# Kernel tuning notes

Hardware: AMD Instinct MI355X
Metric: run time of the kernel (lower is better)

The kernel has to match this reference:

```python
import jax, jax.numpy as jnp
import numpy as np

H = 768
R = 7  # len(DISCOURSE_RELATIONS)


def setup_inputs() -> dict:
    key = jax.random.key(0)
    ks = jax.random.split(key, 6)
    B, S = 4, 256
    scale = 1.0 / np.sqrt(H)
    return {
        "pooled_outputs": jax.random.normal(ks[0], (B, S, H), dtype=jnp.float32),
        "w_src": jax.random.uniform(ks[1], (H, H), jnp.float32, -scale, scale),
        "b_src": jax.random.uniform(ks[2], (H,), jnp.float32, -scale, scale),
        "w_tgt": jax.random.uniform(ks[3], (H, H), jnp.float32, -scale, scale),
        "b_tgt": jax.random.uniform(ks[4], (H,), jnp.float32, -scale, scale),
        "w_out": jax.random.uniform(ks[5], (R, H), jnp.float32, -scale, scale),
    }


def reference(pooled_outputs, w_src, b_src, w_tgt, b_tgt, w_out):
    # h_src, h_tgt: [B, S, H]
    h_src = jnp.einsum("bsh,kh->bsk", pooled_outputs, w_src) + b_src
    h_tgt = jnp.einsum("bth,kh->btk", pooled_outputs, w_tgt) + b_tgt
    # broadcast add -> [B, S, S, H], tanh, then small-output linear -> [B, S, S, R]
    h = jnp.tanh(h_src[:, :, None, :] + h_tgt[:, None, :, :])
    return jnp.einsum("bsth,rh->bstr", h, w_out)
```

## Files before the change

kernel.cpp:

```cpp
#include <hip/hip_runtime.h>
#include <hip/hip_bf16.h>

#define HD 768
#define SQ 256
#define NB 4
#define RR 7

typedef short bf16x8 __attribute__((ext_vector_type(8)));
typedef float f32x4  __attribute__((ext_vector_type(4)));

__device__ __forceinline__ float fast_tanh(float x) {
  float e = __expf(2.0f * x);
  return 1.0f - 2.0f / (e + 1.0f);
}

__device__ __forceinline__ float pair_tanh(float a, float b) {
  return (a + b) * __builtin_amdgcn_rcpf(fmaf(a, b, 1.0f));
}

__device__ __forceinline__ short f2bf(float x) {
  return (short)__builtin_bit_cast(unsigned short, __float2bfloat16(x));
}

__device__ __forceinline__ void gl_lds16(const void* g, void* l) {
  __builtin_amdgcn_global_load_lds(
      (const __attribute__((address_space(1))) void*)g,
      (__attribute__((address_space(3))) void*)l, 16, 0, 0);
}

__global__ __launch_bounds__(256) void cvt_kernel(
    const float* __restrict__ X, const float* __restrict__ Ws,
    const float* __restrict__ Wt, const float* __restrict__ Wo,
    short* __restrict__ Xb, short* __restrict__ Wsb,
    short* __restrict__ Wtb, short* __restrict__ Wob)
{
  const int NX = NB * SQ * HD / 8;
  const int NW = HD * HD / 8;
  const int NO = 16 * HD / 8;
  int i = blockIdx.x * 256 + threadIdx.x;
  const float* src; short* dst;
  if (i < NX)               { src = X;  dst = Xb; }
  else if (i < NX + NW)     { src = Ws; dst = Wsb; i -= NX; }
  else if (i < NX + 2 * NW) { src = Wt; dst = Wtb; i -= NX + NW; }
  else if (i < NX + 2 * NW + NO) {
    i -= NX + 2 * NW;
    int row = i / (HD / 8);
    bf16x8 r = {};
    if (row < RR) {
      float4 a = *(const float4*)(Wo + (size_t)i * 8);
      float4 b = *(const float4*)(Wo + (size_t)i * 8 + 4);
      r[0] = f2bf(a.x); r[1] = f2bf(a.y); r[2] = f2bf(a.z); r[3] = f2bf(a.w);
      r[4] = f2bf(b.x); r[5] = f2bf(b.y); r[6] = f2bf(b.z); r[7] = f2bf(b.w);
    }
    *(bf16x8*)(Wob + (size_t)i * 8) = r;
    return;
  } else return;
  float4 a = *(const float4*)(src + (size_t)i * 8);
  float4 b = *(const float4*)(src + (size_t)i * 8 + 4);
  bf16x8 r;
  r[0] = f2bf(a.x); r[1] = f2bf(a.y); r[2] = f2bf(a.z); r[3] = f2bf(a.w);
  r[4] = f2bf(b.x); r[5] = f2bf(b.y); r[6] = f2bf(b.z); r[7] = f2bf(b.w);
  *(bf16x8*)(dst + (size_t)i * 8) = r;
}

__global__ __launch_bounds__(256) void cvt_wout(
    const float* __restrict__ Wo, short* __restrict__ Wob)
{
  const int NO = 16 * HD / 8;
  int i = blockIdx.x * 256 + threadIdx.x;
  if (i >= NO) return;
  int row = i / (HD / 8);
  bf16x8 r = {};
  if (row < RR) {
    float4 a = *(const float4*)(Wo + (size_t)i * 8);
    float4 b = *(const float4*)(Wo + (size_t)i * 8 + 4);
    r[0] = f2bf(a.x); r[1] = f2bf(a.y); r[2] = f2bf(a.z); r[3] = f2bf(a.w);
    r[4] = f2bf(b.x); r[5] = f2bf(b.y); r[6] = f2bf(b.z); r[7] = f2bf(b.w);
  }
  *(bf16x8*)(Wob + (size_t)i * 8) = r;
}

__global__ __launch_bounds__(256) void stage1_lds(
    const short* __restrict__ Xb,
    const short* __restrict__ Wsb, const float* __restrict__ bsrc,
    const short* __restrict__ Wtb, const float* __restrict__ btgt,
    float* __restrict__ ta, float* __restrict__ tb)
{
  constexpr int BK = 64, BM = 32, BN = 64;
  const short* W  = blockIdx.z ? Wtb : Wsb;
  const float* bv = blockIdx.z ? btgt : bsrc;
  float* outp     = blockIdx.z ? tb : ta;
  const int row0 = blockIdx.x * BM, col0 = blockIdx.y * BN;

  __shared__ short As[2][BM * BK];
  __shared__ short Bs[2][BN * BK];

  const int tid = threadIdx.x, wave = tid >> 6, lane = tid & 63;
  const int ln = lane & 15, lg = lane >> 4;
  const int wm = (wave >> 1) * 16, wn = (wave & 1) * 32;

  f32x4 acc[2] = {};

  const int ra = tid >> 3, ga = tid & 7;
  const size_t xoff = (size_t)(row0 + ra) * HD + ((ga ^ (ra & 7)) * 8);
  const int rb0 = tid >> 3, gb0 = tid & 7;
  const int rb1 = (tid + 256) >> 3, gb1 = tid & 7;
  const size_t wof0 = (size_t)(col0 + rb0) * HD + ((gb0 ^ (rb0 & 7)) * 8);
  const size_t wof1 = (size_t)(col0 + rb1) * HD + ((gb1 ^ (rb1 & 7)) * 8);
  short* const laA  = (short*)As + (size_t)(wave * 64) * 8;
  short* const laB0 = (short*)Bs + (size_t)(wave * 64) * 8;
  short* const laB1 = (short*)Bs + (size_t)(256 + wave * 64) * 8;
  constexpr int BUFA = BM * BK, BUFB = BN * BK;

  gl_lds16(Xb + xoff, laA);
  gl_lds16(W + wof0, laB0);
  gl_lds16(W + wof1, laB1);

  int cur = 0;
  for (int k0 = 0; k0 < HD; k0 += BK) {
    __syncthreads();
    if (k0 + BK < HD) {
      gl_lds16(Xb + xoff + k0 + BK, laA + (cur ^ 1) * BUFA);
      gl_lds16(W + wof0 + k0 + BK, laB0 + (cur ^ 1) * BUFB);
      gl_lds16(W + wof1 + k0 + BK, laB1 + (cur ^ 1) * BUFB);
    }
    const short* Ac = (const short*)As + cur * BUFA;
    const short* Bc = (const short*)Bs + cur * BUFB;

    #pragma unroll
    for (int kkb = 0; kkb < 2; ++kkb) {
      const int q = kkb * 4 + lg;
      const int ar = wm + ln;
      bf16x8 af = *(const bf16x8*)&Ac[ar * BK + ((q ^ (ar & 7)) * 8)];
      bf16x8 bw[2];
      #pragma unroll
      for (int i = 0; i < 2; ++i) {
        int br = wn + i * 16 + ln;
        bw[i] = *(const bf16x8*)&Bc[br * BK + ((q ^ (br & 7)) * 8)];
      }
      #pragma unroll
      for (int i = 0; i < 2; ++i)
        acc[i] = __builtin_amdgcn_mfma_f32_16x16x32_bf16(af, bw[i], acc[i], 0, 0, 0);
    }
    cur ^= 1;
  }

  #pragma unroll
  for (int j = 0; j < 2; ++j) {
    int n = col0 + wn + j * 16 + ln;
    float bb = bv[n];
    #pragma unroll
    for (int r = 0; r < 4; ++r) {
      int m = row0 + wm + lg * 4 + r;
      outp[(size_t)m * HD + n] = fast_tanh(acc[j][r] + bb);
    }
  }
}

__global__ __launch_bounds__(256) void stage1_mfma(
    const float* __restrict__ X,
    const float* __restrict__ Wsrc, const float* __restrict__ bsrc,
    const float* __restrict__ Wtgt, const float* __restrict__ btgt,
    float* __restrict__ ta, float* __restrict__ tb)
{
  constexpr int BK = 64;
  const float* W  = blockIdx.z ? Wtgt : Wsrc;
  const float* bv = blockIdx.z ? btgt : bsrc;
  float* outp     = blockIdx.z ? tb : ta;
  const int row0 = blockIdx.x * 64, col0 = blockIdx.y * 64;

  __shared__ short As[64 * BK];
  __shared__ short Bs[64 * BK];

  const int tid  = threadIdx.x;
  const int wave = tid >> 6, lane = tid & 63;
  const int wm = (wave >> 1) * 32, wn = (wave & 1) * 32;
  f32x4 acc[2][2] = {};
  const int sr = tid >> 2, sq = tid & 3;

  for (int k0 = 0; k0 < HD; k0 += BK) {
    const float* xa = X + (size_t)(row0 + sr) * HD + k0 + sq * 16;
    const float* xw = W + (size_t)(col0 + sr) * HD + k0 + sq * 16;
    float4 a0 = *(const float4*)(xa + 0), a1 = *(const float4*)(xa + 4);
    float4 a2 = *(const float4*)(xa + 8), a3 = *(const float4*)(xa + 12);
    float4 w0 = *(const float4*)(xw + 0), w1 = *(const float4*)(xw + 4);
    float4 w2 = *(const float4*)(xw + 8), w3 = *(const float4*)(xw + 12);
    __syncthreads();
    bf16x8 p;
    p[0]=f2bf(a0.x);p[1]=f2bf(a0.y);p[2]=f2bf(a0.z);p[3]=f2bf(a0.w);
    p[4]=f2bf(a1.x);p[5]=f2bf(a1.y);p[6]=f2bf(a1.z);p[7]=f2bf(a1.w);
    *(bf16x8*)&As[sr * BK + (((sq * 2 + 0) ^ (sr & 7)) * 8)] = p;
    p[0]=f2bf(a2.x);p[1]=f2bf(a2.y);p[2]=f2bf(a2.z);p[3]=f2bf(a2.w);
    p[4]=f2bf(a3.x);p[5]=f2bf(a3.y);p[6]=f2bf(a3.z);p[7]=f2bf(a3.w);
    *(bf16x8*)&As[sr * BK + (((sq * 2 + 1) ^ (sr & 7)) * 8)] = p;
    p[0]=f2bf(w0.x);p[1]=f2bf(w0.y);p[2]=f2bf(w0.z);p[3]=f2bf(w0.w);
    p[4]=f2bf(w1.x);p[5]=f2bf(w1.y);p[6]=f2bf(w1.z);p[7]=f2bf(w1.w);
    *(bf16x8*)&Bs[sr * BK + (((sq * 2 + 0) ^ (sr & 7)) * 8)] = p;
    p[0]=f2bf(w2.x);p[1]=f2bf(w2.y);p[2]=f2bf(w2.z);p[3]=f2bf(w2.w);
    p[4]=f2bf(w3.x);p[5]=f2bf(w3.y);p[6]=f2bf(w3.z);p[7]=f2bf(w3.w);
    *(bf16x8*)&Bs[sr * BK + (((sq * 2 + 1) ^ (sr & 7)) * 8)] = p;
    __syncthreads();

    #pragma unroll
    for (int kkb = 0; kkb < 2; ++kkb) {
      bf16x8 af[2], bw[2];
      const int q = kkb * 4 + (lane >> 4);
      #pragma unroll
      for (int i = 0; i < 2; ++i) {
        int ar = wm + i * 16 + (lane & 15);
        af[i] = *(const bf16x8*)&As[ar * BK + ((q ^ (ar & 7)) * 8)];
        int br = wn + i * 16 + (lane & 15);
        bw[i] = *(const bf16x8*)&Bs[br * BK + ((q ^ (br & 7)) * 8)];
      }
      #pragma unroll
      for (int i = 0; i < 2; ++i)
        #pragma unroll
        for (int j = 0; j < 2; ++j)
          acc[i][j] = __builtin_amdgcn_mfma_f32_16x16x32_bf16(af[i], bw[j], acc[i][j], 0, 0, 0);
    }
  }

  #pragma unroll
  for (int j = 0; j < 2; ++j) {
    int n = col0 + wn + j * 16 + (lane & 15);
    float bb = bv[n];
    #pragma unroll
    for (int i = 0; i < 2; ++i)
      #pragma unroll
      for (int r = 0; r < 4; ++r) {
        int m = row0 + wm + i * 16 + (lane >> 4) * 4 + r;
        outp[(size_t)m * HD + n] = fast_tanh(acc[i][j][r] + bb);
      }
  }
}

__global__ __launch_bounds__(256, 5) void stage2_mfma(
    const float* __restrict__ ta, const float* __restrict__ tb,
    const short* __restrict__ Wob, float* __restrict__ out)
{
  constexpr int HC = 128, LDp = 132, NC = HD / HC;
  const int b  = blockIdx.z;
  const int s0 = blockIdx.y * 8, t0 = blockIdx.x * 16;

  __shared__ float sa[8][LDp];
  __shared__ float sb[16][LDp];

  const int tid = threadIdx.x, wave = tid >> 6, lane = tid & 63;
  const int lg = lane >> 4;
  const int ln = lane & 15;

  f32x4 acc[2] = {};

  const float* taB = ta + ((size_t)b * SQ + s0) * HD;
  const float* tbB = tb + ((size_t)b * SQ + t0) * HD;
  const short* wrow = Wob + (size_t)ln * HD + lg * 8;

  const int sr = tid >> 5, sq = tid & 31;
  const int rba = tid >> 5;

  float4 va  = *(const float4*)(taB + (size_t)sr * HD + sq * 4);
  float4 vb0 = *(const float4*)(tbB + (size_t)rba * HD + sq * 4);
  float4 vb1 = *(const float4*)(tbB + (size_t)(rba + 8) * HD + sq * 4);
  bf16x8 bfr[4], bfrN[4];
  #pragma unroll
  for (int m = 0; m < 4; ++m)
    bfr[m] = *(const bf16x8*)(wrow + m * 32);

  #pragma unroll
  for (int c = 0; c < NC; ++c) {
    *(float4*)&sa[sr][sq * 4]       = va;
    *(float4*)&sb[rba][sq * 4]      = vb0;
    *(float4*)&sb[rba + 8][sq * 4]  = vb1;
    __syncthreads();

    if (c + 1 < NC) {
      va  = *(const float4*)(taB + (size_t)sr * HD + (c + 1) * HC + sq * 4);
      vb0 = *(const float4*)(tbB + (size_t)rba * HD + (c + 1) * HC + sq * 4);
      vb1 = *(const float4*)(tbB + (size_t)(rba + 8) * HD + (c + 1) * HC + sq * 4);
      #pragma unroll
      for (int m = 0; m < 4; ++m)
        bfrN[m] = *(const bf16x8*)(wrow + (c + 1) * HC + m * 32);
    }

    #pragma unroll
    for (int m = 0; m < 4; ++m) {
      const int kk = m * 32 + lg * 8;
      float4 q0 = *(const float4*)&sb[ln][kk];
      float4 q1 = *(const float4*)&sb[ln][kk + 4];
      float bvv[8] = {q0.x,q0.y,q0.z,q0.w,q1.x,q1.y,q1.z,q1.w};

      #pragma unroll
      for (int si = 0; si < 2; ++si) {
        const float* ap = &sa[wave * 2 + si][kk];
        float4 a0 = *(const float4*)ap;
        float4 a1 = *(const float4*)(ap + 4);
        float av[8] = {a0.x,a0.y,a0.z,a0.w,a1.x,a1.y,a1.z,a1.w};
        bf16x8 pa;
        #pragma unroll
        for (int j = 0; j < 8; ++j)
          pa[j] = f2bf(pair_tanh(av[j], bvv[j]));
        acc[si] = __builtin_amdgcn_mfma_f32_16x16x32_bf16(pa, bfr[m], acc[si], 0, 0, 0);
      }
    }
    __syncthreads();
    if (c + 1 < NC) {
      #pragma unroll
      for (int m = 0; m < 4; ++m)
        bfr[m] = bfrN[m];
    }
  }

  if (ln < RR) {
    #pragma unroll
    for (int si = 0; si < 2; ++si) {
      int s = s0 + wave * 2 + si;
      float* op = out + (((size_t)b * SQ + s) * SQ + t0 + lg * 4) * RR + ln;
      op[0]      = acc[si][0];
      op[RR]     = acc[si][1];
      op[2 * RR] = acc[si][2];
      op[3 * RR] = acc[si][3];
    }
  }
}

extern "C" void kernel_launch(void* const* d_in, const int* in_sizes, int n_in,
                              void* d_out, int out_size, void* d_ws, size_t ws_size,
                              hipStream_t stream) {
  (void)in_sizes; (void)n_in; (void)out_size;
  const float* X    = (const float*)d_in[0];
  const float* Wsrc = (const float*)d_in[1];
  const float* bsrc = (const float*)d_in[2];
  const float* Wtgt = (const float*)d_in[3];
  const float* btgt = (const float*)d_in[4];
  const float* Wout = (const float*)d_in[5];
  float* out = (float*)d_out;

  float* taF = (float*)d_ws;
  float* tbF = taF + (size_t)NB * SQ * HD;
  const size_t base = (size_t)2 * NB * SQ * HD * sizeof(float);
  short* Xb  = (short*)((char*)d_ws + base);
  short* Wsb = Xb + (size_t)NB * SQ * HD;
  short* Wtb = Wsb + (size_t)HD * HD;
  short* Wob = Wtb + (size_t)HD * HD;
  const size_t need = base +
      ((size_t)NB * SQ * HD + 2 * (size_t)HD * HD + (size_t)16 * HD) * sizeof(short);

  const short* WobUse;
  if (ws_size >= need) {
    const int total_oct = NB*SQ*HD/8 + 2*(HD*HD/8) + 16*HD/8;
    cvt_kernel<<<(total_oct + 255) / 256, 256, 0, stream>>>(
        X, Wsrc, Wtgt, Wout, Xb, Wsb, Wtb, Wob);
    stage1_lds<<<dim3(32, 12, 2), 256, 0, stream>>>(Xb, Wsb, bsrc, Wtb, btgt, taF, tbF);
    WobUse = Wob;
  } else {
    short* WobF = (short*)((char*)d_ws + base);
    cvt_wout<<<6, 256, 0, stream>>>(Wout, WobF);
    stage1_mfma<<<dim3(16, 12, 2), 256, 0, stream>>>(X, Wsrc, bsrc, Wtgt, btgt, taF, tbF);
    WobUse = WobF;
  }
  stage2_mfma<<<dim3(SQ / 16, SQ / 8, NB), 256, 0, stream>>>(taF, tbF, WobUse, out);
}
```

Measured before the change: 114.8 us.

## Double stage2 H-chunk, load W_out per step, vectorize pair-tanh as float2

Doubles the per-iteration H chunk in stage2 from 128 to 256, so there are fewer chunk iterations and block barriers. The W_out bf16 fragments are now loaded directly inside each step instead of being prefetched into register buffers. The pair-tanh arithmetic is rewritten with float2 vectors so the compiler can emit packed FP32 add and multiply instructions. The cost is about double the LDS per block, which may reduce occupancy below the launch-bounds target of 5, and W_out load latency is no longer hidden by prefetch.

```diff
diff --git a/kernel.cpp b/kernel.cpp
--- a/kernel.cpp
+++ b/kernel.cpp
@@ -8,14 +8,11 @@
 
 typedef short bf16x8 __attribute__((ext_vector_type(8)));
 typedef float f32x4  __attribute__((ext_vector_type(4)));
+typedef float f32x2  __attribute__((ext_vector_type(2)));
 
 __device__ __forceinline__ float fast_tanh(float x) {
   float e = __expf(2.0f * x);
   return 1.0f - 2.0f / (e + 1.0f);
-}
-
-__device__ __forceinline__ float pair_tanh(float a, float b) {
-  return (a + b) * __builtin_amdgcn_rcpf(fmaf(a, b, 1.0f));
 }
 
 __device__ __forceinline__ short f2bf(float x) {
@@ -238,7 +235,7 @@
     const float* __restrict__ ta, const float* __restrict__ tb,
     const short* __restrict__ Wob, float* __restrict__ out)
 {
-  constexpr int HC = 128, LDp = 132, NC = HD / HC;
+  constexpr int HC = 256, LDp = 260, NC = HD / HC;
   const int b  = blockIdx.z;
   const int s0 = blockIdx.y * 8, t0 = blockIdx.x * 16;
 
@@ -256,58 +253,64 @@
   const short* wrow = Wob + (size_t)ln * HD + lg * 8;
 
   const int sr = tid >> 5, sq = tid & 31;
-  const int rba = tid >> 5;
-
-  float4 va  = *(const float4*)(taB + (size_t)sr * HD + sq * 4);
-  float4 vb0 = *(const float4*)(tbB + (size_t)rba * HD + sq * 4);
-  float4 vb1 = *(const float4*)(tbB + (size_t)(rba + 8) * HD + sq * 4);
-  bf16x8 bfr[4], bfrN[4];
-  #pragma unroll
-  for (int m = 0; m < 4; ++m)
-    bfr[m] = *(const bf16x8*)(wrow + m * 32);
-
-  #pragma unroll
+
+  float4 va0  = *(const float4*)(taB + (size_t)sr * HD + sq * 4);
+  float4 va1  = *(const float4*)(taB + (size_t)sr * HD + sq * 4 + 128);
+  float4 vb00 = *(const float4*)(tbB + (size_t)sr * HD + sq * 4);
+  float4 vb01 = *(const float4*)(tbB + (size_t)sr * HD + sq * 4 + 128);
+  float4 vb10 = *(const float4*)(tbB + (size_t)(sr + 8) * HD + sq * 4);
+  float4 vb11 = *(const float4*)(tbB + (size_t)(sr + 8) * HD + sq * 4 + 128);
+
   for (int c = 0; c < NC; ++c) {
-    *(float4*)&sa[sr][sq * 4]       = va;
-    *(float4*)&sb[rba][sq * 4]      = vb0;
-    *(float4*)&sb[rba + 8][sq * 4]  = vb1;
+    *(float4*)&sa[sr][sq * 4]            = va0;
+    *(float4*)&sa[sr][sq * 4 + 128]      = va1;
+    *(float4*)&sb[sr][sq * 4]            = vb00;
+    *(float4*)&sb[sr][sq * 4 + 128]      = vb01;
+    *(float4*)&sb[sr + 8][sq * 4]        = vb10;
+    *(float4*)&sb[sr + 8][sq * 4 + 128]  = vb11;
     __syncthreads();
 
     if (c + 1 < NC) {
-      va  = *(const float4*)(taB + (size_t)sr * HD + (c + 1) * HC + sq * 4);
-      vb0 = *(const float4*)(tbB + (size_t)rba * HD + (c + 1) * HC + sq * 4);
-      vb1 = *(const float4*)(tbB + (size_t)(rba + 8) * HD + (c + 1) * HC + sq * 4);
-      #pragma unroll
-      for (int m = 0; m < 4; ++m)
-        bfrN[m] = *(const bf16x8*)(wrow + (c + 1) * HC + m * 32);
-    }
-
-    #pragma unroll
-    for (int m = 0; m < 4; ++m) {
+      const float* tap = taB + (size_t)sr * HD + (c + 1) * HC + sq * 4;
+      const float* tbp = tbB + (size_t)sr * HD + (c + 1) * HC + sq * 4;
+      va0  = *(const float4*)tap;
+      va1  = *(const float4*)(tap + 128);
+      vb00 = *(const float4*)tbp;
+      vb01 = *(const float4*)(tbp + 128);
+      vb10 = *(const float4*)(tbp + (size_t)8 * HD);
+      vb11 = *(const float4*)(tbp + (size_t)8 * HD + 128);
+    }
+
+    #pragma unroll
+    for (int m = 0; m < HC / 32; ++m) {
       const int kk = m * 32 + lg * 8;
+      bf16x8 bfr = *(const bf16x8*)(wrow + c * HC + m * 32);
       float4 q0 = *(const float4*)&sb[ln][kk];
       float4 q1 = *(const float4*)&sb[ln][kk + 4];
-      float bvv[8] = {q0.x,q0.y,q0.z,q0.w,q1.x,q1.y,q1.z,q1.w};
+      f32x2 bv2[4] = {{q0.x, q0.y}, {q0.z, q0.w}, {q1.x, q1.y}, {q1.z, q1.w}};
 
       #pragma unroll
       for (int si = 0; si < 2; ++si) {
         const float* ap = &sa[wave * 2 + si][kk];
         float4 a0 = *(const float4*)ap;
         float4 a1 = *(const float4*)(ap + 4);
-        float av[8] = {a0.x,a0.y,a0.z,a0.w,a1.x,a1.y,a1.z,a1.w};
+        f32x2 av2[4] = {{a0.x, a0.y}, {a0.z, a0.w}, {a1.x, a1.y}, {a1.z, a1.w}};
         bf16x8 pa;
         #pragma unroll
-        for (int j = 0; j < 8; ++j)
-          pa[j] = f2bf(pair_tanh(av[j], bvv[j]));
-        acc[si] = __builtin_amdgcn_mfma_f32_16x16x32_bf16(pa, bfr[m], acc[si], 0, 0, 0);
+        for (int j = 0; j < 4; ++j) {
+          f32x2 s = av2[j] + bv2[j];
+          f32x2 d = av2[j] * bv2[j] + (f32x2){1.0f, 1.0f};
+          f32x2 r;
+          r[0] = __builtin_amdgcn_rcpf(d[0]);
+          r[1] = __builtin_amdgcn_rcpf(d[1]);
+          f32x2 res = s * r;
+          pa[2 * j]     = f2bf(res[0]);
+          pa[2 * j + 1] = f2bf(res[1]);
+        }
+        acc[si] = __builtin_amdgcn_mfma_f32_16x16x32_bf16(pa, bfr, acc[si], 0, 0, 0);
       }
     }
     __syncthreads();
-    if (c + 1 < NC) {
-      #pragma unroll
-      for (int m = 0; m < 4; ++m)
-        bfr[m] = bfrN[m];
-    }
   }
 
   if (ln < RR) {
```

Measured after the change: 115.7 us. About the same (+0.8%).

## Drop LDS staging in stage2 and read operands directly from global memory

Applied to the files above, without the earlier changes.

Stage2 no longer stages ta/tb tiles through shared memory with double-buffered register prefetch and block barriers. Each lane now loads its A rows, B row and W_out fragment straight from global memory (relying on L1/L2) inside a single unrolled K loop. This removes the LDS traffic and the __syncthreads calls, and occupancy is raised to 6 blocks per SM. The cost is redundant global/cache loads across waves (the tb rows are re-read by all four waves) and less explicit latency hiding.

```diff
diff --git a/kernel.cpp b/kernel.cpp
--- a/kernel.cpp
+++ b/kernel.cpp
@@ -234,16 +234,12 @@
   }
 }
 
-__global__ __launch_bounds__(256, 5) void stage2_mfma(
+__global__ __launch_bounds__(256, 6) void stage2_mfma(
     const float* __restrict__ ta, const float* __restrict__ tb,
     const short* __restrict__ Wob, float* __restrict__ out)
 {
-  constexpr int HC = 128, LDp = 132, NC = HD / HC;
   const int b  = blockIdx.z;
   const int s0 = blockIdx.y * 8, t0 = blockIdx.x * 16;
-
-  __shared__ float sa[8][LDp];
-  __shared__ float sb[16][LDp];
 
   const int tid = threadIdx.x, wave = tid >> 6, lane = tid & 63;
   const int lg = lane >> 4;
@@ -251,62 +247,30 @@
 
   f32x4 acc[2] = {};
 
-  const float* taB = ta + ((size_t)b * SQ + s0) * HD;
-  const float* tbB = tb + ((size_t)b * SQ + t0) * HD;
-  const short* wrow = Wob + (size_t)ln * HD + lg * 8;
-
-  const int sr = tid >> 5, sq = tid & 31;
-  const int rba = tid >> 5;
-
-  float4 va  = *(const float4*)(taB + (size_t)sr * HD + sq * 4);
-  float4 vb0 = *(const float4*)(tbB + (size_t)rba * HD + sq * 4);
-  float4 vb1 = *(const float4*)(tbB + (size_t)(rba + 8) * HD + sq * 4);
-  bf16x8 bfr[4], bfrN[4];
-  #pragma unroll
-  for (int m = 0; m < 4; ++m)
-    bfr[m] = *(const bf16x8*)(wrow + m * 32);
-
-  #pragma unroll
-  for (int c = 0; c < NC; ++c) {
-    *(float4*)&sa[sr][sq * 4]       = va;
-    *(float4*)&sb[rba][sq * 4]      = vb0;
-    *(float4*)&sb[rba + 8][sq * 4]  = vb1;
-    __syncthreads();
-
-    if (c + 1 < NC) {
-      va  = *(const float4*)(taB + (size_t)sr * HD + (c + 1) * HC + sq * 4);
-      vb0 = *(const float4*)(tbB + (size_t)rba * HD + (c + 1) * HC + sq * 4);
-      vb1 = *(const float4*)(tbB + (size_t)(rba + 8) * HD + (c + 1) * HC + sq * 4);
-      #pragma unroll
-      for (int m = 0; m < 4; ++m)
-        bfrN[m] = *(const bf16x8*)(wrow + (c + 1) * HC + m * 32);
-    }
-
-    #pragma unroll
-    for (int m = 0; m < 4; ++m) {
-      const int kk = m * 32 + lg * 8;
-      float4 q0 = *(const float4*)&sb[ln][kk];
-      float4 q1 = *(const float4*)&sb[ln][kk + 4];
-      float bvv[8] = {q0.x,q0.y,q0.z,q0.w,q1.x,q1.y,q1.z,q1.w};
-
-      #pragma unroll
-      for (int si = 0; si < 2; ++si) {
-        const float* ap = &sa[wave * 2 + si][kk];
-        float4 a0 = *(const float4*)ap;
-        float4 a1 = *(const float4*)(ap + 4);
-        float av[8] = {a0.x,a0.y,a0.z,a0.w,a1.x,a1.y,a1.z,a1.w};
-        bf16x8 pa;
-        #pragma unroll
-        for (int j = 0; j < 8; ++j)
-          pa[j] = f2bf(pair_tanh(av[j], bvv[j]));
-        acc[si] = __builtin_amdgcn_mfma_f32_16x16x32_bf16(pa, bfr[m], acc[si], 0, 0, 0);
-      }
-    }
-    __syncthreads();
-    if (c + 1 < NC) {
-      #pragma unroll
-      for (int m = 0; m < 4; ++m)
-        bfr[m] = bfrN[m];
+  const float* a0p = ta + ((size_t)b * SQ + s0 + wave * 2 + 0) * HD + lg * 8;
+  const float* a1p = ta + ((size_t)b * SQ + s0 + wave * 2 + 1) * HD + lg * 8;
+  const float* bp  = tb + ((size_t)b * SQ + t0 + ln) * HD + lg * 8;
+  const short* wp  = Wob + (size_t)ln * HD + lg * 8;
+
+  #pragma unroll 4
+  for (int m = 0; m < HD / 32; ++m) {
+    const int kk = m * 32;
+    bf16x8 bfr = *(const bf16x8*)(wp + kk);
+    float4 q0 = *(const float4*)(bp + kk);
+    float4 q1 = *(const float4*)(bp + kk + 4);
+    float bvv[8] = {q0.x,q0.y,q0.z,q0.w,q1.x,q1.y,q1.z,q1.w};
+
+    #pragma unroll
+    for (int si = 0; si < 2; ++si) {
+      const float* ap = si ? a1p : a0p;
+      float4 a0 = *(const float4*)(ap + kk);
+      float4 a1 = *(const float4*)(ap + kk + 4);
+      float av[8] = {a0.x,a0.y,a0.z,a0.w,a1.x,a1.y,a1.z,a1.w};
+      bf16x8 pa;
+      #pragma unroll
+      for (int j = 0; j < 8; ++j)
+        pa[j] = f2bf(pair_tanh(av[j], bvv[j]));
+      acc[si] = __builtin_amdgcn_mfma_f32_16x16x32_bf16(pa, bfr, acc[si], 0, 0, 0);
     }
   }
 
```

Result: slower. 171.6 us (+49.4%).
